# Kernel tuning notes

Measured on AMD Instinct MI355X. Metric: run time of the kernel, lower is better.

The kernel has to match this reference:

```python
import jax, jax.numpy as jnp
import numpy as np

D_IN, D, P, H, DH, DFF, L = 3072, 1024, 36, 8, 128, 2048, 6
SCALE = np.float32(1.0 / np.sqrt(DH))
# leave-one-out index matrix: row i lists all patch indices except i -> (36, 35)
LOO_IDX = jnp.asarray(np.array([[j for j in range(P) if j != i] for i in range(P)], dtype=np.int32))


def _ln(x, g, b, eps=1e-5):
    m = jnp.mean(x, axis=-1, keepdims=True)
    v = jnp.var(x, axis=-1, keepdims=True)
    return (x - m) / jnp.sqrt(v + eps) * g + b


def setup_inputs() -> dict:
    key = jax.random.key(0)
    ks = jax.random.split(key, 16)
    w = lambda k, shape: jax.random.normal(k, shape, jnp.float32) * 0.02
    return {
        "x": jax.random.normal(ks[0], (128, P, D_IN), jnp.float32),
        "ln0_g": jnp.ones((D_IN,), jnp.float32), "ln0_b": jnp.zeros((D_IN,), jnp.float32),
        "Wred": w(ks[1], (D, D_IN)), "bred": jnp.zeros((D,), jnp.float32),
        "h0_w1": w(ks[2], (64, D)), "h0_b1": jnp.zeros((64,), jnp.float32),
        "h0_w2": w(ks[3], (1, 64)), "h0_b2": jnp.zeros((1,), jnp.float32),
        "temperature": jnp.ones((1,), jnp.float32) * 0.07,
        "Wqkv": w(ks[4], (L, 3 * D, D)), "bqkv": jnp.zeros((L, 3 * D), jnp.float32),
        "Wo": w(ks[5], (L, D, D)), "bo": jnp.zeros((L, D), jnp.float32),
        "ln1_g": jnp.ones((L, D), jnp.float32), "ln1_b": jnp.zeros((L, D), jnp.float32),
        "W1": w(ks[6], (L, DFF, D)), "b1": jnp.zeros((L, DFF), jnp.float32),
        "W2": w(ks[7], (L, D, DFF)), "b2": jnp.zeros((L, D), jnp.float32),
        "ln2_g": jnp.ones((L, D), jnp.float32), "ln2_b": jnp.zeros((L, D), jnp.float32),
        "lnf_g": jnp.ones((D,), jnp.float32), "lnf_b": jnp.zeros((D,), jnp.float32),
    }


def reference(x, ln0_g, ln0_b, Wred, bred, h0_w1, h0_b1, h0_w2, h0_b2, temperature,
              Wqkv, bqkv, Wo, bo, ln1_g, ln1_b, W1, b1, W2, b2, ln2_g, ln2_b, lnf_g, lnf_b):
    B = x.shape[0]
    # dim_reduce (dropout is identity at inference)
    xr = jax.nn.gelu(_ln(x, ln0_g, ln0_b) @ Wred.T + bred, approximate=False)  # (B,P,D)

    # Leave-one-out attention maps. H0 is a pointwise (kernel_size=1) stack,
    # so each position's score is independent: compute once, then gather the
    h1 = jax.nn.gelu(jnp.einsum('bpc,oc->bpo', xr, h0_w1) + h0_b1, approximate=False)  # (B,P,64)
    full = jnp.einsum('bpo,uo->bpu', h1, h0_w2)[..., 0] + h0_b2[0]                      # (B,P)
    attention_maps = jax.nn.sigmoid(full[:, LOO_IDX] / temperature[0])                  # (B,P,P-1)

    # Pre-norm transformer encoder (PyTorch norm_first=True, relu FFN, no final encoder norm)
    y = xr
    for l in range(L):
        qkv = _ln(y, ln1_g[l], ln1_b[l]) @ Wqkv[l].T + bqkv[l]  # (B,P,3D)
        q, k, v = jnp.split(qkv, 3, axis=-1)
        q = q.reshape(B, P, H, DH).transpose(0, 2, 1, 3)
        k = k.reshape(B, P, H, DH).transpose(0, 2, 1, 3)
        v = v.reshape(B, P, H, DH).transpose(0, 2, 1, 3)
        attn = jax.nn.softmax(jnp.einsum('bhqd,bhkd->bhqk', q, k) * SCALE, axis=-1)
        o = jnp.einsum('bhqk,bhkd->bhqd', attn, v).transpose(0, 2, 1, 3).reshape(B, P, D)
        y = y + o @ Wo[l].T + bo[l]
        f = jax.nn.relu(_ln(y, ln2_g[l], ln2_b[l]) @ W1[l].T + b1[l])
        y = y + f @ W2[l].T + b2[l]

    return _ln(y, lnf_g, lnf_b), attention_maps
```

## Files before the change

kernel.cpp:

```cpp
#include <hip/hip_runtime.h>
#include <hip/hip_bf16.h>

typedef unsigned short u16;
typedef unsigned int u32;
typedef __bf16 bf16x8 __attribute__((ext_vector_type(8)));
typedef float f32x4 __attribute__((ext_vector_type(4)));

#define DEV static __device__ __forceinline__
#define GPTR(p) (const __attribute__((address_space(1))) u32*)(p)
#define LPTR(p) (__attribute__((address_space(3))) u32*)(p)

DEV float bf2f(u16 u) { return __uint_as_float((u32)u << 16); }
DEV u16 f2bf(float f) {
  u32 x = __float_as_uint(f);
  x += 0x7fffu + ((x >> 16) & 1u);
  return (u16)(x >> 16);
}
DEV u32 pk2(float a, float b) { return (u32)f2bf(a) | ((u32)f2bf(b) << 16); }
DEV float gelu_f(float x) { return 0.5f * x * (1.0f + erff(x * 0.70710678118654752440f)); }

__global__ void cvt5_k(const float* __restrict__ s0, const float* __restrict__ s1,
                       const float* __restrict__ s2, const float* __restrict__ s3,
                       const float* __restrict__ s4,
                       u16* __restrict__ d0, u16* __restrict__ d1, u16* __restrict__ d2,
                       u16* __restrict__ d3, u16* __restrict__ d4,
                       int n0, int n1, int n2, int n3, int n4) {
  const int total = n0 + n1 + n2 + n3 + n4;
  for (int i = blockIdx.x * 256 + threadIdx.x; i < total; i += gridDim.x * 256) {
    const float* s; u16* d; int j = i;
    if (j < n0) { s = s0; d = d0; }
    else {
      j -= n0;
      if (j < n1) { s = s1; d = d1; }
      else {
        j -= n1;
        if (j < n2) { s = s2; d = d2; }
        else {
          j -= n2;
          if (j < n3) { s = s3; d = d3; }
          else { j -= n3; s = s4; d = d4; }
        }
      }
    }
    float4 a = ((const float4*)s)[j * 2];
    float4 b = ((const float4*)s)[j * 2 + 1];
    uint4 o;
    o.x = pk2(a.x, a.y); o.y = pk2(a.z, a.w);
    o.z = pk2(b.x, b.y); o.w = pk2(b.z, b.w);
    ((uint4*)d)[j] = o;
  }
}

__global__ void w1t_k(const float* __restrict__ w1, float* __restrict__ w1t) {
  int i = blockIdx.x * 256 + threadIdx.x;
  if (i < 64 * 1024) {
    int o = i >> 10, c = i & 1023;
    w1t[c * 64 + o] = w1[i];
  }
}

template<int DIM, int OUTM, int INBF>
__global__ __launch_bounds__(256) void ln_k(const void* __restrict__ inp,
                                            const float* __restrict__ g,
                                            const float* __restrict__ b,
                                            void* __restrict__ outp) {
  constexpr int NG = DIM / 512;
  const int w = threadIdx.x >> 6, lane = threadIdx.x & 63;
  const int row = blockIdx.x * 4 + w;
  float v[NG * 8];
  if (INBF == 1) {
    const u16* in = (const u16*)inp + (size_t)row * DIM;
#pragma unroll
    for (int i = 0; i < NG; ++i) {
      uint4 u = ((const uint4*)in)[i * 64 + lane];
      const u16* e = (const u16*)&u;
#pragma unroll
      for (int t = 0; t < 8; ++t) v[i * 8 + t] = bf2f(e[t]);
    }
  } else {
    const float* in = (const float*)inp + (size_t)row * DIM;
#pragma unroll
    for (int i = 0; i < NG; ++i)
#pragma unroll
      for (int h = 0; h < 2; ++h) {
        float4 f = ((const float4*)in)[i * 128 + h * 64 + lane];
        v[i * 8 + h * 4 + 0] = f.x; v[i * 8 + h * 4 + 1] = f.y;
        v[i * 8 + h * 4 + 2] = f.z; v[i * 8 + h * 4 + 3] = f.w;
      }
  }
  float s = 0.f, s2 = 0.f;
#pragma unroll
  for (int t = 0; t < NG * 8; ++t) { s += v[t]; s2 += v[t] * v[t]; }
#pragma unroll
  for (int d = 1; d < 64; d <<= 1) { s += __shfl_xor(s, d); s2 += __shfl_xor(s2, d); }
  const float mean = s / DIM;
  const float rstd = rsqrtf(s2 / DIM - mean * mean + 1e-5f);

  if (INBF == 1) {
#pragma unroll
    for (int i = 0; i < NG; ++i) {
      const int u8 = i * 64 + lane;
      float o[8];
#pragma unroll
      for (int h = 0; h < 2; ++h) {
        float4 gv = ((const float4*)g)[u8 * 2 + h];
        float4 bv = ((const float4*)b)[u8 * 2 + h];
        o[h * 4 + 0] = (v[i * 8 + h * 4 + 0] - mean) * rstd * gv.x + bv.x;
        o[h * 4 + 1] = (v[i * 8 + h * 4 + 1] - mean) * rstd * gv.y + bv.y;
        o[h * 4 + 2] = (v[i * 8 + h * 4 + 2] - mean) * rstd * gv.z + bv.z;
        o[h * 4 + 3] = (v[i * 8 + h * 4 + 3] - mean) * rstd * gv.w + bv.w;
      }
      if (OUTM == 0) {
        uint4 u;
        u.x = pk2(o[0], o[1]); u.y = pk2(o[2], o[3]);
        u.z = pk2(o[4], o[5]); u.w = pk2(o[6], o[7]);
        ((uint4*)((u16*)outp + (size_t)row * DIM))[u8] = u;
      } else {
        float* orow = (float*)outp + (size_t)row * DIM;
#pragma unroll
        for (int h = 0; h < 2; ++h)
          ((float4*)orow)[u8 * 2 + h] =
              make_float4(o[h * 4 + 0], o[h * 4 + 1], o[h * 4 + 2], o[h * 4 + 3]);
      }
    }
  } else {
#pragma unroll
    for (int i = 0; i < NG; ++i) {
#pragma unroll
      for (int h = 0; h < 2; ++h) {
        const int u4 = i * 128 + h * 64 + lane;
        float4 gv = ((const float4*)g)[u4];
        float4 bv = ((const float4*)b)[u4];
        float o0 = (v[i * 8 + h * 4 + 0] - mean) * rstd * gv.x + bv.x;
        float o1 = (v[i * 8 + h * 4 + 1] - mean) * rstd * gv.y + bv.y;
        float o2 = (v[i * 8 + h * 4 + 2] - mean) * rstd * gv.z + bv.z;
        float o3 = (v[i * 8 + h * 4 + 3] - mean) * rstd * gv.w + bv.w;
        if (OUTM == 0) {
          ushort4 u;
          u.x = f2bf(o0); u.y = f2bf(o1); u.z = f2bf(o2); u.w = f2bf(o3);
          ((ushort4*)((u16*)outp + (size_t)row * DIM))[u4] = u;
        } else {
          ((float4*)((float*)outp + (size_t)row * DIM))[u4] = make_float4(o0, o1, o2, o3);
        }
      }
    }
  }
}

template<int EPI, int BN>
__global__ __launch_bounds__(512, BN == 64 ? 6 : 4)
void gemm_bt(const u16* __restrict__ A,
             const u16* __restrict__ B,
             const float* __restrict__ bias,
             u16* __restrict__ Cb,
             int N, int K, int nx) {
  constexpr int WC = BN / 32;
  constexpr int MR = (128 * WC / 8) / 16;
  __shared__ u16 As[2][128 * 64];
  __shared__ u16 Bs[2][BN * 64];
  const int tid = threadIdx.x;
  const int nwg = gridDim.x;
  const int bid = blockIdx.x;
  const int swz = (bid & 7) * (nwg >> 3) + (bid >> 3);
  const int by = swz / nx, bx = swz - by * nx;
  const int brow = by * 128, bcol = bx * BN;
  const int lane = tid & 63, w = tid >> 6;
  const int wr = (w / WC) * (MR * 16), wc = (w % WC) * 32;
  const int fr = lane & 15, fg = lane >> 4;
  const int swb = (fr & 7) << 4;
  const int ldr = lane >> 3;
  const int lc8 = lane & 7;
  const int cs8 = (lc8 ^ ldr) * 8;

  const u16* Ab = A + (size_t)(brow + ldr) * K + cs8;
  const u16* Bb = B + (size_t)(bcol + ldr) * K + cs8;

  f32x4 acc[MR][2];
  const f32x4 z = {0.f, 0.f, 0.f, 0.f};
#pragma unroll
  for (int m = 0; m < MR; ++m) { acc[m][0] = z; acc[m][1] = z; }

  auto stage = [&](int kt, int buf) {
    const int k0 = kt << 6;
#pragma unroll
    for (int i = 0; i < 2; ++i) {
      const int c = i * 8 + w;
      __builtin_amdgcn_global_load_lds(GPTR(Ab + (size_t)c * 8 * K + k0),
                                       LPTR(&As[buf][c * 512 + lane * 8]), 16, 0, 0);
    }
#pragma unroll
    for (int i = 0; i < BN / 64; ++i) {
      const int c = i * 8 + w;
      __builtin_amdgcn_global_load_lds(GPTR(Bb + (size_t)c * 8 * K + k0),
                                       LPTR(&Bs[buf][c * 512 + lane * 8]), 16, 0, 0);
    }
  };

  stage(0, 0);
  const int nkt = K >> 6;
  for (int kt = 0; kt < nkt; ++kt) {
    const int buf = kt & 1;
    asm volatile("s_waitcnt vmcnt(0)" ::: "memory");
    __builtin_amdgcn_s_barrier();
    __builtin_amdgcn_sched_barrier(0);
    if (kt + 1 < nkt) stage(kt + 1, buf ^ 1);
    const char* Asb = (const char*)&As[buf][0];
    const char* Bsb = (const char*)&Bs[buf][0];
    __builtin_amdgcn_s_setprio(1);
#pragma unroll
    for (int ks = 0; ks < 2; ++ks) {
      bf16x8 af[MR], bfr[2];
      const int cb = (ks * 64 + fg * 16) ^ swb;
#pragma unroll
      for (int m = 0; m < MR; ++m)
        af[m] = *(const bf16x8*)(Asb + (wr + m * 16 + fr) * 128 + cb);
#pragma unroll
      for (int n = 0; n < 2; ++n)
        bfr[n] = *(const bf16x8*)(Bsb + (wc + n * 16 + fr) * 128 + cb);
#pragma unroll
      for (int m = 0; m < MR; ++m)
#pragma unroll
        for (int n = 0; n < 2; ++n)
          acc[m][n] = __builtin_amdgcn_mfma_f32_16x16x32_bf16(af[m], bfr[n], acc[m][n], 0, 0, 0);
    }
    __builtin_amdgcn_s_setprio(0);
  }

#pragma unroll
  for (int n = 0; n < 2; ++n) {
    const int col = bcol + wc + n * 16 + fr;
    const float bv = bias[col];
#pragma unroll
    for (int m = 0; m < MR; ++m) {
      const int row0 = brow + wr + m * 16 + fg * 4;
#pragma unroll
      for (int j = 0; j < 4; ++j) {
        float v = acc[m][n][j] + bv;
        const size_t idx = (size_t)(row0 + j) * N + col;
        if (EPI == 0) Cb[idx] = f2bf(gelu_f(v));
        else if (EPI == 1) Cb[idx] = f2bf(v);
        else if (EPI == 2) Cb[idx] = f2bf(bf2f(Cb[idx]) + v);
        else Cb[idx] = f2bf(fmaxf(v, 0.f));
      }
    }
  }
}

__global__ __launch_bounds__(128) void attn_k(const u16* __restrict__ qkv,
                                              u16* __restrict__ o) {
  __shared__ u16 lds[2][12672];
  const int tid = threadIdx.x, w = tid >> 6, l = tid & 63;
  const int b = blockIdx.x >> 2, hp = blockIdx.x & 3;
  const int h = hp * 2 + w;
  u16* Vt = &lds[w][0];
  u16* P  = &lds[w][9216];
  const int fr = l & 15, fg = l >> 4;
  const size_t qbase = (size_t)b * 36 * 3072 + h * 128;
  const size_t kbase = qbase + 1024;
  const size_t vbase = qbase + 2048;

  for (int i = l; i < 1584; i += 64) {
    uint4 zz = {0u, 0u, 0u, 0u};
    *(uint4*)&lds[w][i * 8] = zz;
  }

  for (int i = l; i < 576; i += 64) {
    const int k = i >> 4, nc = (i & 15) * 8;
    uint4 u = *(const uint4*)&qkv[vbase + (size_t)k * 3072 + nc];
    const u16* e = (const u16*)&u;
#pragma unroll
    for (int t = 0; t < 8; ++t) Vt[(nc + t) * 72 + k] = e[t];
  }

  const f32x4 z = {0.f, 0.f, 0.f, 0.f};
  f32x4 S[3][3];
#pragma unroll
  for (int mt = 0; mt < 3; ++mt)
#pragma unroll
    for (int nt = 0; nt < 3; ++nt) S[mt][nt] = z;
#pragma unroll
  for (int ks = 0; ks < 4; ++ks) {
    bf16x8 qa[3], kb[3];
#pragma unroll
    for (int mt = 0; mt < 3; ++mt) {
      const int r = min(mt * 16 + fr, 35);
      qa[mt] = *(const bf16x8*)&qkv[qbase + (size_t)r * 3072 + ks * 32 + fg * 8];
      kb[mt] = *(const bf16x8*)&qkv[kbase + (size_t)r * 3072 + ks * 32 + fg * 8];
    }
#pragma unroll
    for (int mt = 0; mt < 3; ++mt)
#pragma unroll
      for (int nt = 0; nt < 3; ++nt)
        S[mt][nt] = __builtin_amdgcn_mfma_f32_16x16x32_bf16(qa[mt], kb[nt], S[mt][nt], 0, 0, 0);
  }

  const float sc = 0.08838834764831845f;
#pragma unroll
  for (int mt = 0; mt < 3; ++mt) {
#pragma unroll
    for (int j = 0; j < 4; ++j) {
      float v0 = S[mt][0][j] * sc;
      float v1 = S[mt][1][j] * sc;
      float v2 = (fr >= 4) ? -1e30f : S[mt][2][j] * sc;
      float m = fmaxf(fmaxf(v0, v1), v2);
#pragma unroll
      for (int d = 1; d < 16; d <<= 1) m = fmaxf(m, __shfl_xor(m, d));
      float e0 = __expf(v0 - m);
      float e1 = __expf(v1 - m);
      float e2 = (fr >= 4) ? 0.f : __expf(v2 - m);
      float sum = e0 + e1 + e2;
#pragma unroll
      for (int d = 1; d < 16; d <<= 1) sum += __shfl_xor(sum, d);
      const float inv = 1.f / sum;
      const int r = mt * 16 + fg * 4 + j;
      P[r * 72 + fr]      = f2bf(e0 * inv);
      P[r * 72 + 16 + fr] = f2bf(e1 * inv);
      P[r * 72 + 32 + fr] = f2bf(e2 * inv);
    }
  }

#pragma unroll
  for (int g = 0; g < 2; ++g) {
    f32x4 O[3][4];
#pragma unroll
    for (int mt = 0; mt < 3; ++mt)
#pragma unroll
      for (int nt = 0; nt < 4; ++nt) O[mt][nt] = z;
#pragma unroll
    for (int ks = 0; ks < 2; ++ks) {
      bf16x8 pa[3], vb[4];
#pragma unroll
      for (int mt = 0; mt < 3; ++mt)
        pa[mt] = *(const bf16x8*)&P[(mt * 16 + fr) * 72 + ks * 32 + fg * 8];
#pragma unroll
      for (int nt = 0; nt < 4; ++nt)
        vb[nt] = *(const bf16x8*)&Vt[((g * 4 + nt) * 16 + fr) * 72 + ks * 32 + fg * 8];
#pragma unroll
      for (int mt = 0; mt < 3; ++mt)
#pragma unroll
        for (int nt = 0; nt < 4; ++nt)
          O[mt][nt] = __builtin_amdgcn_mfma_f32_16x16x32_bf16(pa[mt], vb[nt], O[mt][nt], 0, 0, 0);
    }
#pragma unroll
    for (int mt = 0; mt < 3; ++mt) {
#pragma unroll
      for (int j = 0; j < 4; ++j) {
        const int r = mt * 16 + fg * 4 + j;
        if (r < 36) {
#pragma unroll
          for (int nt = 0; nt < 4; ++nt)
            o[((size_t)b * 36 + r) * 1024 + h * 128 + g * 64 + nt * 16 + fr] =
                f2bf(O[mt][nt][j]);
        }
      }
    }
  }
}

__global__ __launch_bounds__(256) void h0_k(const u16* __restrict__ xr,
                                            const float* __restrict__ w1t,
                                            const float* __restrict__ b1,
                                            const float* __restrict__ w2,
                                            const float* __restrict__ b2v,
                                            float* __restrict__ full) {
  __shared__ float xs[8][1024];
  const int t0 = blockIdx.x * 8, tid = threadIdx.x;
#pragma unroll
  for (int i = 0; i < 8; ++i) {
    const int idx = tid + i * 256;
    const int t = idx >> 8, c4 = idx & 255;
    ushort4 u = ((const ushort4*)(xr + (size_t)(t0 + t) * 1024))[c4];
    xs[t][c4 * 4 + 0] = bf2f(u.x);
    xs[t][c4 * 4 + 1] = bf2f(u.y);
    xs[t][c4 * 4 + 2] = bf2f(u.z);
    xs[t][c4 * 4 + 3] = bf2f(u.w);
  }
  __syncthreads();
  const int w = tid >> 6, lane = tid & 63;
  float s0 = 0.f, s1 = 0.f;
  for (int c = 0; c < 1024; ++c) {
    const float wv = w1t[c * 64 + lane];
    s0 = fmaf(xs[w * 2 + 0][c], wv, s0);
    s1 = fmaf(xs[w * 2 + 1][c], wv, s1);
  }
  const float bb = b1[lane], wo = w2[lane];
  float v0 = gelu_f(s0 + bb) * wo;
  float v1 = gelu_f(s1 + bb) * wo;
#pragma unroll
  for (int off = 32; off; off >>= 1) {
    v0 += __shfl_down(v0, off);
    v1 += __shfl_down(v1, off);
  }
  if (lane == 0) {
    full[t0 + w * 2 + 0] = v0 + b2v[0];
    full[t0 + w * 2 + 1] = v1 + b2v[0];
  }
}

__global__ void am2_k(const float* __restrict__ full, const float* __restrict__ temp,
                      float* __restrict__ out) {
  const int i = blockIdx.x * 256 + threadIdx.x;
  if (i < 128 * 36 * 35) {
    const int j = i % 35;
    const int t = i / 35;
    const int p = t % 36;
    const int b = t / 36;
    const int col = j + (j >= p ? 1 : 0);
    const float v = full[b * 36 + col] / temp[0];
    out[i] = 1.f / (1.f + expf(-v));
  }
}

extern "C" void kernel_launch(void* const* d_in, const int* in_sizes, int n_in,
                              void* d_out, int out_size, void* d_ws, size_t ws_size,
                              hipStream_t stream) {
  const float* x     = (const float*)d_in[0];
  const float* ln0_g = (const float*)d_in[1];
  const float* ln0_b = (const float*)d_in[2];
  const float* Wred  = (const float*)d_in[3];
  const float* bred  = (const float*)d_in[4];
  const float* h0_w1 = (const float*)d_in[5];
  const float* h0_b1 = (const float*)d_in[6];
  const float* h0_w2 = (const float*)d_in[7];
  const float* h0_b2 = (const float*)d_in[8];
  const float* temp  = (const float*)d_in[9];
  const float* Wqkv  = (const float*)d_in[10];
  const float* bqkv  = (const float*)d_in[11];
  const float* Wo    = (const float*)d_in[12];
  const float* bo    = (const float*)d_in[13];
  const float* ln1_g = (const float*)d_in[14];
  const float* ln1_b = (const float*)d_in[15];
  const float* W1    = (const float*)d_in[16];
  const float* b1    = (const float*)d_in[17];
  const float* W2    = (const float*)d_in[18];
  const float* b2    = (const float*)d_in[19];
  const float* ln2_g = (const float*)d_in[20];
  const float* ln2_b = (const float*)d_in[21];
  const float* lnf_g = (const float*)d_in[22];
  const float* lnf_b = (const float*)d_in[23];

  char* ws = (char*)d_ws;
  size_t off = 0;
  auto alloc = [&](size_t bytes) -> void* {
    void* p = ws + off;
    off += (bytes + 255) & ~(size_t)255;
    return p;
  };
  u16* WredB  = (u16*)alloc((size_t)1024 * 3072 * 2);
  u16* WqkvB  = (u16*)alloc((size_t)6 * 3072 * 1024 * 2);
  u16* WoB    = (u16*)alloc((size_t)6 * 1024 * 1024 * 2);
  u16* W1B    = (u16*)alloc((size_t)6 * 2048 * 1024 * 2);
  u16* W2B    = (u16*)alloc((size_t)6 * 1024 * 2048 * 2);
  float* w1t  = (float*)alloc((size_t)1024 * 64 * 4);
  u16* yb     = (u16*)alloc((size_t)4608 * 1024 * 2);
  u16* big    = (u16*)alloc((size_t)4608 * 3072 * 2);
  u16* nbuf   = (u16*)alloc((size_t)4608 * 1024 * 2);
  float* fullb = (float*)alloc((size_t)4608 * 4);

  cvt5_k<<<3072, 256, 0, stream>>>(
      Wred, Wqkv, Wo, W1, W2, WredB, WqkvB, WoB, W1B, W2B,
      (int)(1024 * 3072 / 8), (int)(6 * 3072 * 1024 / 8), (int)(6 * 1024 * 1024 / 8),
      (int)(6 * 2048 * 1024 / 8), (int)(6 * 1024 * 2048 / 8));
  w1t_k<<<64 * 1024 / 256, 256, 0, stream>>>(h0_w1, w1t);

  ln_k<3072, 0, 0><<<1152, 256, 0, stream>>>(x, ln0_g, ln0_b, big);
  gemm_bt<0, 64><<<16 * 36, 512, 0, stream>>>(big, WredB, bred, yb, 1024, 3072, 16);
  h0_k<<<576, 256, 0, stream>>>(yb, w1t, h0_b1, h0_w2, h0_b2, fullb);
  am2_k<<<(128 * 36 * 35 + 255) / 256, 256, 0, stream>>>(fullb, temp,
                                                         (float*)d_out + 4608 * 1024);

  for (int l = 0; l < 6; ++l) {
    ln_k<1024, 0, 1><<<1152, 256, 0, stream>>>(yb, ln1_g + l * 1024, ln1_b + l * 1024, nbuf);
    gemm_bt<1, 128><<<24 * 36, 512, 0, stream>>>(nbuf, WqkvB + (size_t)l * 3072 * 1024,
                                                 bqkv + l * 3072, big, 3072, 1024, 24);
    attn_k<<<128 * 4, 128, 0, stream>>>(big, nbuf);
    gemm_bt<2, 64><<<16 * 36, 512, 0, stream>>>(nbuf, WoB + (size_t)l * 1024 * 1024,
                                                bo + l * 1024, yb, 1024, 1024, 16);
    ln_k<1024, 0, 1><<<1152, 256, 0, stream>>>(yb, ln2_g + l * 1024, ln2_b + l * 1024, nbuf);
    gemm_bt<3, 128><<<16 * 36, 512, 0, stream>>>(nbuf, W1B + (size_t)l * 2048 * 1024,
                                                 b1 + l * 2048, big, 2048, 1024, 16);
    gemm_bt<2, 64><<<16 * 36, 512, 0, stream>>>(big, W2B + (size_t)l * 1024 * 2048,
                                                b2 + l * 1024, yb, 1024, 2048, 16);
  }
  ln_k<1024, 1, 1><<<1152, 256, 0, stream>>>(yb, lnf_g, lnf_b, d_out);
}
```

Before: 1.126 ms.

## Add two-wave 128x64 GEMM kernel for N=1024 projections; nontemporal weight-convert loads

Adds a new gemm2w kernel that computes a 128x64 output tile with only two waves (128 threads). Each wave owns a 64x64 sub-tile with 4x4 MFMA accumulators, using double-buffered LDS filled by direct global-to-LDS loads. The dim-reduce, Wo and W2 GEMMs (N=1024) now use it instead of the 512-thread gemm_bt, aiming for more register-level reuse per wave and less barrier overhead, at the cost of fewer waves per tile to hide latency. The weight-conversion kernel also switches to nontemporal loads so the one-time fp32 weight reads do not pollute the cache.

```diff
diff --git a/kernel.cpp b/kernel.cpp
--- a/kernel.cpp
+++ b/kernel.cpp
@@ -42,11 +42,11 @@
         }
       }
     }
-    float4 a = ((const float4*)s)[j * 2];
-    float4 b = ((const float4*)s)[j * 2 + 1];
+    f32x4 a = __builtin_nontemporal_load((const f32x4*)s + j * 2);
+    f32x4 b = __builtin_nontemporal_load((const f32x4*)s + j * 2 + 1);
     uint4 o;
-    o.x = pk2(a.x, a.y); o.y = pk2(a.z, a.w);
-    o.z = pk2(b.x, b.y); o.w = pk2(b.z, b.w);
+    o.x = pk2(a[0], a[1]); o.y = pk2(a[2], a[3]);
+    o.z = pk2(b[0], b[1]); o.w = pk2(b[2], b[3]);
     ((uint4*)d)[j] = o;
   }
 }
@@ -233,6 +233,102 @@
 #pragma unroll
     for (int m = 0; m < MR; ++m) {
       const int row0 = brow + wr + m * 16 + fg * 4;
+#pragma unroll
+      for (int j = 0; j < 4; ++j) {
+        float v = acc[m][n][j] + bv;
+        const size_t idx = (size_t)(row0 + j) * N + col;
+        if (EPI == 0) Cb[idx] = f2bf(gelu_f(v));
+        else if (EPI == 1) Cb[idx] = f2bf(v);
+        else if (EPI == 2) Cb[idx] = f2bf(bf2f(Cb[idx]) + v);
+        else Cb[idx] = f2bf(fmaxf(v, 0.f));
+      }
+    }
+  }
+}
+
+template<int EPI>
+__global__ __launch_bounds__(128, 2)
+void gemm2w(const u16* __restrict__ A,
+            const u16* __restrict__ B,
+            const float* __restrict__ bias,
+            u16* __restrict__ Cb,
+            int N, int K, int nx) {
+  __shared__ u16 As[2][128 * 64];
+  __shared__ u16 Bs[2][64 * 64];
+  const int tid = threadIdx.x;
+  const int nwg = gridDim.x, bid = blockIdx.x;
+  const int swz = (bid & 7) * (nwg >> 3) + (bid >> 3);
+  const int by = swz / nx, bx = swz - by * nx;
+  const int brow = by * 128, bcol = bx * 64;
+  const int lane = tid & 63, w = tid >> 6;
+  const int fr = lane & 15, fg = lane >> 4;
+  const int swb = (fr & 7) << 4;
+  const int ldr = lane >> 3;
+  const int cs8 = ((lane & 7) ^ ldr) * 8;
+
+  const u16* Ab = A + (size_t)(brow + ldr) * K + cs8;
+  const u16* Bb = B + (size_t)(bcol + ldr) * K + cs8;
+
+  f32x4 acc[4][4];
+  const f32x4 z = {0.f, 0.f, 0.f, 0.f};
+#pragma unroll
+  for (int m = 0; m < 4; ++m)
+#pragma unroll
+    for (int n = 0; n < 4; ++n) acc[m][n] = z;
+
+  auto stage = [&](int kt, int buf) {
+    const int k0 = kt << 6;
+#pragma unroll
+    for (int i = 0; i < 8; ++i) {
+      const int g = i * 2 + w;
+      __builtin_amdgcn_global_load_lds(GPTR(Ab + (size_t)(g * 8) * K + k0),
+                                       LPTR(&As[buf][g * 512 + lane * 8]), 16, 0, 0);
+    }
+#pragma unroll
+    for (int i = 0; i < 4; ++i) {
+      const int g = i * 2 + w;
+      __builtin_amdgcn_global_load_lds(GPTR(Bb + (size_t)(g * 8) * K + k0),
+                                       LPTR(&Bs[buf][g * 512 + lane * 8]), 16, 0, 0);
+    }
+  };
+
+  stage(0, 0);
+  const int nkt = K >> 6;
+  for (int kt = 0; kt < nkt; ++kt) {
+    const int buf = kt & 1;
+    asm volatile("s_waitcnt vmcnt(0)" ::: "memory");
+    __builtin_amdgcn_s_barrier();
+    __builtin_amdgcn_sched_barrier(0);
+    if (kt + 1 < nkt) stage(kt + 1, buf ^ 1);
+    const char* Asb = (const char*)&As[buf][0];
+    const char* Bsb = (const char*)&Bs[buf][0];
+    __builtin_amdgcn_s_setprio(1);
+#pragma unroll
+    for (int ks = 0; ks < 2; ++ks) {
+      bf16x8 af[4], bfr[4];
+      const int cb = (ks * 64 + fg * 16) ^ swb;
+#pragma unroll
+      for (int m = 0; m < 4; ++m)
+        af[m] = *(const bf16x8*)(Asb + (w * 64 + m * 16 + fr) * 128 + cb);
+#pragma unroll
+      for (int n = 0; n < 4; ++n)
+        bfr[n] = *(const bf16x8*)(Bsb + (n * 16 + fr) * 128 + cb);
+#pragma unroll
+      for (int m = 0; m < 4; ++m)
+#pragma unroll
+        for (int n = 0; n < 4; ++n)
+          acc[m][n] = __builtin_amdgcn_mfma_f32_16x16x32_bf16(af[m], bfr[n], acc[m][n], 0, 0, 0);
+    }
+    __builtin_amdgcn_s_setprio(0);
+  }
+
+#pragma unroll
+  for (int n = 0; n < 4; ++n) {
+    const int col = bcol + n * 16 + fr;
+    const float bv = bias[col];
+#pragma unroll
+    for (int m = 0; m < 4; ++m) {
+      const int row0 = brow + w * 64 + m * 16 + fg * 4;
 #pragma unroll
       for (int j = 0; j < 4; ++j) {
         float v = acc[m][n][j] + bv;
@@ -464,7 +560,7 @@
   w1t_k<<<64 * 1024 / 256, 256, 0, stream>>>(h0_w1, w1t);
 
   ln_k<3072, 0, 0><<<1152, 256, 0, stream>>>(x, ln0_g, ln0_b, big);
-  gemm_bt<0, 64><<<16 * 36, 512, 0, stream>>>(big, WredB, bred, yb, 1024, 3072, 16);
+  gemm2w<0><<<36 * 16, 128, 0, stream>>>(big, WredB, bred, yb, 1024, 3072, 16);
   h0_k<<<576, 256, 0, stream>>>(yb, w1t, h0_b1, h0_w2, h0_b2, fullb);
   am2_k<<<(128 * 36 * 35 + 255) / 256, 256, 0, stream>>>(fullb, temp,
                                                          (float*)d_out + 4608 * 1024);
@@ -474,13 +570,13 @@
     gemm_bt<1, 128><<<24 * 36, 512, 0, stream>>>(nbuf, WqkvB + (size_t)l * 3072 * 1024,
                                                  bqkv + l * 3072, big, 3072, 1024, 24);
     attn_k<<<128 * 4, 128, 0, stream>>>(big, nbuf);
-    gemm_bt<2, 64><<<16 * 36, 512, 0, stream>>>(nbuf, WoB + (size_t)l * 1024 * 1024,
-                                                bo + l * 1024, yb, 1024, 1024, 16);
+    gemm2w<2><<<36 * 16, 128, 0, stream>>>(nbuf, WoB + (size_t)l * 1024 * 1024,
+                                           bo + l * 1024, yb, 1024, 1024, 16);
     ln_k<1024, 0, 1><<<1152, 256, 0, stream>>>(yb, ln2_g + l * 1024, ln2_b + l * 1024, nbuf);
     gemm_bt<3, 128><<<16 * 36, 512, 0, stream>>>(nbuf, W1B + (size_t)l * 2048 * 1024,
                                                  b1 + l * 2048, big, 2048, 1024, 16);
-    gemm_bt<2, 64><<<16 * 36, 512, 0, stream>>>(big, W2B + (size_t)l * 1024 * 2048,
-                                                b2 + l * 1024, yb, 1024, 2048, 16);
+    gemm2w<2><<<36 * 16, 128, 0, stream>>>(big, W2B + (size_t)l * 1024 * 2048,
+                                           b2 + l * 1024, yb, 1024, 2048, 16);
   }
   ln_k<1024, 1, 1><<<1152, 256, 0, stream>>>(yb, lnf_g, lnf_b, d_out);
 }
```

Measured after the change: 1.219 ms. 1.08x slower.

## Fuse fp32-to-bf16 weight conversion into GEMM B-tile loading

Applied to the files above, without the earlier changes.

Drops the separate kernel that converted all fp32 weights to bf16 up front. The GEMM now loads fp32 weight tiles into registers, converts them to bf16, and writes them to LDS after the MFMA compute, double-buffered against the next iteration. This removes a full pass over roughly 100M weight elements and its bf16 writeback. In exchange each GEMM tile reads twice the weight bytes, and because weight tiles are shared across many M-blocks the fp32 weights are re-read and re-converted many times. The B path also no longer uses asynchronous direct-to-LDS loads, so register pressure rises.

```diff
diff --git a/kernel.cpp b/kernel.cpp
--- a/kernel.cpp
+++ b/kernel.cpp
@@ -18,38 +18,6 @@
 }
 DEV u32 pk2(float a, float b) { return (u32)f2bf(a) | ((u32)f2bf(b) << 16); }
 DEV float gelu_f(float x) { return 0.5f * x * (1.0f + erff(x * 0.70710678118654752440f)); }
-
-__global__ void cvt5_k(const float* __restrict__ s0, const float* __restrict__ s1,
-                       const float* __restrict__ s2, const float* __restrict__ s3,
-                       const float* __restrict__ s4,
-                       u16* __restrict__ d0, u16* __restrict__ d1, u16* __restrict__ d2,
-                       u16* __restrict__ d3, u16* __restrict__ d4,
-                       int n0, int n1, int n2, int n3, int n4) {
-  const int total = n0 + n1 + n2 + n3 + n4;
-  for (int i = blockIdx.x * 256 + threadIdx.x; i < total; i += gridDim.x * 256) {
-    const float* s; u16* d; int j = i;
-    if (j < n0) { s = s0; d = d0; }
-    else {
-      j -= n0;
-      if (j < n1) { s = s1; d = d1; }
-      else {
-        j -= n1;
-        if (j < n2) { s = s2; d = d2; }
-        else {
-          j -= n2;
-          if (j < n3) { s = s3; d = d3; }
-          else { j -= n3; s = s4; d = d4; }
-        }
-      }
-    }
-    float4 a = ((const float4*)s)[j * 2];
-    float4 b = ((const float4*)s)[j * 2 + 1];
-    uint4 o;
-    o.x = pk2(a.x, a.y); o.y = pk2(a.z, a.w);
-    o.z = pk2(b.x, b.y); o.w = pk2(b.z, b.w);
-    ((uint4*)d)[j] = o;
-  }
-}
 
 __global__ void w1t_k(const float* __restrict__ w1, float* __restrict__ w1t) {
   int i = blockIdx.x * 256 + threadIdx.x;
@@ -150,12 +118,13 @@
 template<int EPI, int BN>
 __global__ __launch_bounds__(512, BN == 64 ? 6 : 4)
 void gemm_bt(const u16* __restrict__ A,
-             const u16* __restrict__ B,
+             const float* __restrict__ B,
              const float* __restrict__ bias,
              u16* __restrict__ Cb,
              int N, int K, int nx) {
   constexpr int WC = BN / 32;
   constexpr int MR = (128 * WC / 8) / 16;
+  constexpr int BC = BN / 64;
   __shared__ u16 As[2][128 * 64];
   __shared__ u16 Bs[2][BN * 64];
   const int tid = threadIdx.x;
@@ -173,14 +142,16 @@
   const int cs8 = (lc8 ^ ldr) * 8;
 
   const u16* Ab = A + (size_t)(brow + ldr) * K + cs8;
-  const u16* Bb = B + (size_t)(bcol + ldr) * K + cs8;
+  const float* Bb = B + (size_t)(bcol + ldr) * K + cs8;
 
   f32x4 acc[MR][2];
   const f32x4 z = {0.f, 0.f, 0.f, 0.f};
 #pragma unroll
   for (int m = 0; m < MR; ++m) { acc[m][0] = z; acc[m][1] = z; }
 
-  auto stage = [&](int kt, int buf) {
+  f32x4 breg[BC][2];
+
+  auto stageA = [&](int kt, int buf) {
     const int k0 = kt << 6;
 #pragma unroll
     for (int i = 0; i < 2; ++i) {
@@ -188,22 +159,40 @@
       __builtin_amdgcn_global_load_lds(GPTR(Ab + (size_t)c * 8 * K + k0),
                                        LPTR(&As[buf][c * 512 + lane * 8]), 16, 0, 0);
     }
-#pragma unroll
-    for (int i = 0; i < BN / 64; ++i) {
+  };
+  auto loadB = [&](int kt) {
+    const int k0 = kt << 6;
+#pragma unroll
+    for (int i = 0; i < BC; ++i) {
       const int c = i * 8 + w;
-      __builtin_amdgcn_global_load_lds(GPTR(Bb + (size_t)c * 8 * K + k0),
-                                       LPTR(&Bs[buf][c * 512 + lane * 8]), 16, 0, 0);
+      const float* p = Bb + (size_t)c * 8 * K + k0;
+      breg[i][0] = *(const f32x4*)p;
+      breg[i][1] = *(const f32x4*)(p + 4);
     }
   };
-
-  stage(0, 0);
+  auto writeB = [&](int buf) {
+#pragma unroll
+    for (int i = 0; i < BC; ++i) {
+      const int c = i * 8 + w;
+      uint4 o;
+      o.x = pk2(breg[i][0][0], breg[i][0][1]);
+      o.y = pk2(breg[i][0][2], breg[i][0][3]);
+      o.z = pk2(breg[i][1][0], breg[i][1][1]);
+      o.w = pk2(breg[i][1][2], breg[i][1][3]);
+      *(uint4*)&Bs[buf][c * 512 + lane * 8] = o;
+    }
+  };
+
+  loadB(0);
+  stageA(0, 0);
+  writeB(0);
   const int nkt = K >> 6;
   for (int kt = 0; kt < nkt; ++kt) {
     const int buf = kt & 1;
-    asm volatile("s_waitcnt vmcnt(0)" ::: "memory");
+    asm volatile("s_waitcnt vmcnt(0) lgkmcnt(0)" ::: "memory");
     __builtin_amdgcn_s_barrier();
     __builtin_amdgcn_sched_barrier(0);
-    if (kt + 1 < nkt) stage(kt + 1, buf ^ 1);
+    if (kt + 1 < nkt) { loadB(kt + 1); stageA(kt + 1, buf ^ 1); }
     const char* Asb = (const char*)&As[buf][0];
     const char* Bsb = (const char*)&Bs[buf][0];
     __builtin_amdgcn_s_setprio(1);
@@ -224,6 +213,7 @@
           acc[m][n] = __builtin_amdgcn_mfma_f32_16x16x32_bf16(af[m], bfr[n], acc[m][n], 0, 0, 0);
     }
     __builtin_amdgcn_s_setprio(0);
+    if (kt + 1 < nkt) writeB(buf ^ 1);
   }
 
 #pragma unroll
@@ -446,40 +436,31 @@
     off += (bytes + 255) & ~(size_t)255;
     return p;
   };
-  u16* WredB  = (u16*)alloc((size_t)1024 * 3072 * 2);
-  u16* WqkvB  = (u16*)alloc((size_t)6 * 3072 * 1024 * 2);
-  u16* WoB    = (u16*)alloc((size_t)6 * 1024 * 1024 * 2);
-  u16* W1B    = (u16*)alloc((size_t)6 * 2048 * 1024 * 2);
-  u16* W2B    = (u16*)alloc((size_t)6 * 1024 * 2048 * 2);
   float* w1t  = (float*)alloc((size_t)1024 * 64 * 4);
   u16* yb     = (u16*)alloc((size_t)4608 * 1024 * 2);
   u16* big    = (u16*)alloc((size_t)4608 * 3072 * 2);
   u16* nbuf   = (u16*)alloc((size_t)4608 * 1024 * 2);
   float* fullb = (float*)alloc((size_t)4608 * 4);
 
-  cvt5_k<<<3072, 256, 0, stream>>>(
-      Wred, Wqkv, Wo, W1, W2, WredB, WqkvB, WoB, W1B, W2B,
-      (int)(1024 * 3072 / 8), (int)(6 * 3072 * 1024 / 8), (int)(6 * 1024 * 1024 / 8),
-      (int)(6 * 2048 * 1024 / 8), (int)(6 * 1024 * 2048 / 8));
   w1t_k<<<64 * 1024 / 256, 256, 0, stream>>>(h0_w1, w1t);
 
   ln_k<3072, 0, 0><<<1152, 256, 0, stream>>>(x, ln0_g, ln0_b, big);
-  gemm_bt<0, 64><<<16 * 36, 512, 0, stream>>>(big, WredB, bred, yb, 1024, 3072, 16);
+  gemm_bt<0, 64><<<16 * 36, 512, 0, stream>>>(big, Wred, bred, yb, 1024, 3072, 16);
   h0_k<<<576, 256, 0, stream>>>(yb, w1t, h0_b1, h0_w2, h0_b2, fullb);
   am2_k<<<(128 * 36 * 35 + 255) / 256, 256, 0, stream>>>(fullb, temp,
                                                          (float*)d_out + 4608 * 1024);
 
   for (int l = 0; l < 6; ++l) {
     ln_k<1024, 0, 1><<<1152, 256, 0, stream>>>(yb, ln1_g + l * 1024, ln1_b + l * 1024, nbuf);
-    gemm_bt<1, 128><<<24 * 36, 512, 0, stream>>>(nbuf, WqkvB + (size_t)l * 3072 * 1024,
+    gemm_bt<1, 128><<<24 * 36, 512, 0, stream>>>(nbuf, Wqkv + (size_t)l * 3072 * 1024,
                                                  bqkv + l * 3072, big, 3072, 1024, 24);
     attn_k<<<128 * 4, 128, 0, stream>>>(big, nbuf);
-    gemm_bt<2, 64><<<16 * 36, 512, 0, stream>>>(nbuf, WoB + (size_t)l * 1024 * 1024,
+    gemm_bt<2, 64><<<16 * 36, 512, 0, stream>>>(nbuf, Wo + (size_t)l * 1024 * 1024,
                                                 bo + l * 1024, yb, 1024, 1024, 16);
     ln_k<1024, 0, 1><<<1152, 256, 0, stream>>>(yb, ln2_g + l * 1024, ln2_b + l * 1024, nbuf);
-    gemm_bt<3, 128><<<16 * 36, 512, 0, stream>>>(nbuf, W1B + (size_t)l * 2048 * 1024,
+    gemm_bt<3, 128><<<16 * 36, 512, 0, stream>>>(nbuf, W1 + (size_t)l * 2048 * 1024,
                                                  b1 + l * 2048, big, 2048, 1024, 16);
-    gemm_bt<2, 64><<<16 * 36, 512, 0, stream>>>(big, W2B + (size_t)l * 1024 * 2048,
+    gemm_bt<2, 64><<<16 * 36, 512, 0, stream>>>(big, W2 + (size_t)l * 1024 * 2048,
                                                 b2 + l * 1024, yb, 1024, 2048, 16);
   }
   ln_k<1024, 1, 1><<<1152, 256, 0, stream>>>(yb, lnf_g, lnf_b, d_out);
```

New measurement: 1.377 ms. +22.3%, slower.
